# Kernel optimization log

Hardware: AMD Instinct MI355X
Metric: run time of the kernel (lower is better)

## Reference

```python
import jax, jax.numpy as jnp
import numpy as np

B, C, H, W = 32, 512, 256, 14
NSEL = 7  # 7 even columns (0,2,..,12) on even rows, 7 odd columns (1,3,..,13) on odd rows


def setup_inputs() -> dict:
    key = jax.random.key(0)
    kx, kp = jax.random.split(key)
    x = jax.random.normal(kx, (B, C, H, W), dtype=jnp.float32)
    # per-(batch,row) random permutation of the 7 selected columns
    pkeys = jax.random.split(kp, B * H)
    perms = jax.vmap(lambda k: jax.random.permutation(k, NSEL))(pkeys)
    perms = perms.reshape(B, H, NSEL).astype(jnp.int32)
    return {"x": x, "perms": perms}


def reference(x, perms):
    # Even rows shuffle columns {0,2,...,12}; odd rows shuffle {1,3,...,13}.
    # Column of the j-th selected element on row h: 2*j + (h % 2).
    parity = (jnp.arange(H) % 2).astype(jnp.int32)[None, :, None]      # [1,H,1]
    dst = 2 * jnp.arange(NSEL, dtype=jnp.int32)[None, None, :] + parity  # [1,H,7] -> broadcast [B,H,7]
    dst = jnp.broadcast_to(dst, (B, H, NSEL))
    src = 2 * perms + parity                                            # [B,H,7]
    # Build a per-(b,h) column remap: identity, with dst <- src on shuffled slots.
    colmap = jnp.broadcast_to(jnp.arange(W, dtype=jnp.int32), (B, H, W))
    bi = jnp.arange(B, dtype=jnp.int32)[:, None, None]
    hi = jnp.arange(H, dtype=jnp.int32)[None, :, None]
    colmap = colmap.at[bi, hi, dst].set(src)                            # [B,H,W]
    # Single vectorized gather along the width axis, broadcast over channels.
    idx = jnp.broadcast_to(colmap[:, None, :, :], (B, C, H, W))
    return jnp.take_along_axis(x, idx, axis=3)
```

## Files before the change

### kernel.cpp

```cpp
#include <hip/hip_runtime.h>


#define TILE_ROWS   512
#define TILE_FLOATS (TILE_ROWS * 14)
#define WAVE_ROWS   128
#define WAVE_VEC4   448

#define GLOAD_LDS16(gp, lp)                                                   \
    __builtin_amdgcn_global_load_lds(                                         \
        (const __attribute__((address_space(1))) void*)(gp),                  \
        (__attribute__((address_space(3))) void*)(lp), 16, 0, 0)

__global__ __launch_bounds__(256, 5) void GSRS_shuffle_wave_kernel(
    const float* __restrict__ x,
    const int* __restrict__ perms,
    float* __restrict__ out)
{
    __shared__ float tile[TILE_FLOATS];
    __shared__ unsigned char cmap[256][16];

    const unsigned tid  = threadIdx.x;
    const unsigned lane = tid & 63u;
    const unsigned wv   = tid >> 6;
    const unsigned tb   = blockIdx.x;
    const unsigned base = tb * TILE_FLOATS;
    const unsigned row0 = tb * TILE_ROWS;
    const unsigned b    = row0 >> 17;

    const float4* xv = reinterpret_cast<const float4*>(x + base);
    float4*       tv = reinterpret_cast<float4*>(tile);
    const unsigned q0 = wv * WAVE_VEC4 + lane;
#pragma unroll
    for (int i = 0; i < 7; ++i)
        GLOAD_LDS16(xv + q0 + i * 64, tv + q0 + i * 64);

    {
        const unsigned r0 = wv * WAVE_ROWS + 2u * lane;
        const unsigned h0 = r0 & 255u;
        const int* pr = perms + b * 1792u + h0 * 7u;
        int pm[14];
#pragma unroll
        for (int j = 0; j < 14; ++j) pm[j] = pr[j];
#pragma unroll
        for (int r = 0; r < 2; ++r) {
            const unsigned h = h0 + r;
            const unsigned p = h & 1u;
            union { unsigned char c[16]; uint4 v; } u;
#pragma unroll
            for (int w14 = 0; w14 < 14; ++w14) {
                unsigned src;
                if (((unsigned)w14 & 1u) == p)
                    src = 2u * (unsigned)pm[r * 7 + (w14 >> 1)] + p;
                else
                    src = (unsigned)w14;
                u.c[w14] = (unsigned char)src;
            }
            u.c[14] = 0; u.c[15] = 0;
            *reinterpret_cast<uint4*>(&cmap[h][0]) = u.v;
        }
    }

    asm volatile("s_waitcnt vmcnt(0) lgkmcnt(0)" ::: "memory");

    float4* ov = reinterpret_cast<float4*>(out + base);
#pragma unroll
    for (int i = 0; i < 7; ++i) {
        const unsigned q  = q0 + i * 64;
        unsigned lo   = q * 4u;
        unsigned lrow = lo / 14u;
        unsigned w14  = lo - lrow * 14u;
        float v[4];
#pragma unroll
        for (int k4 = 0; k4 < 4; ++k4) {
            const unsigned h   = lrow & 255u;
            const unsigned src = cmap[h][w14];
            v[k4] = tile[lrow * 14u + src];
            if (++w14 == 14u) { w14 = 0u; ++lrow; }
        }
        ov[q] = make_float4(v[0], v[1], v[2], v[3]);
    }
}

extern "C" void kernel_launch(void* const* d_in, const int* in_sizes, int n_in,
                              void* d_out, int out_size, void* d_ws, size_t ws_size,
                              hipStream_t stream) {
    const float* x     = (const float*)d_in[0];
    const int*   perms = (const int*)d_in[1];
    float*       out   = (float*)d_out;

    hipLaunchKernelGGL(GSRS_shuffle_wave_kernel, dim3(8192), dim3(256), 0, stream,
                       x, perms, out);
}
```

Before: 86.70 us.

## Process four tiles per block with register-prefetched next tile

Each block now handles four consecutive 512-row tiles from the same batch. The next tile is prefetched into registers while the current tile is permuted from LDS and stored. Direct global-to-LDS loads are replaced by ordinary register loads followed by LDS writes, and the column map is built once per block, so per-block setup is amortized and load latency overlaps with the shuffle. The costs are higher register pressure, an extra register-to-LDS write, and a quarter as many blocks, which could hurt latency hiding on a kernel that is already bandwidth-bound.

```diff
diff --git a/kernel.cpp b/kernel.cpp
--- a/kernel.cpp
+++ b/kernel.cpp
@@ -3,15 +3,11 @@
 
 #define TILE_ROWS   512
 #define TILE_FLOATS (TILE_ROWS * 14)
-#define WAVE_ROWS   128
-#define WAVE_VEC4   448
+#define TILE_V4     (TILE_FLOATS / 4)
+#define WAVE_V4     448
+#define TILES_PER_BLOCK 4
 
-#define GLOAD_LDS16(gp, lp)                                                   \
-    __builtin_amdgcn_global_load_lds(                                         \
-        (const __attribute__((address_space(1))) void*)(gp),                  \
-        (__attribute__((address_space(3))) void*)(lp), 16, 0, 0)
-
-__global__ __launch_bounds__(256, 5) void GSRS_shuffle_wave_kernel(
+__global__ __launch_bounds__(256, 5) void GSRS_shuffle_pipe_kernel(
     const float* __restrict__ x,
     const int* __restrict__ perms,
     float* __restrict__ out)
@@ -22,37 +18,36 @@
     const unsigned tid  = threadIdx.x;
     const unsigned lane = tid & 63u;
     const unsigned wv   = tid >> 6;
-    const unsigned tb   = blockIdx.x;
-    const unsigned base = tb * TILE_FLOATS;
-    const unsigned row0 = tb * TILE_ROWS;
-    const unsigned b    = row0 >> 17;
+    const unsigned bid  = blockIdx.x;
+    const unsigned t0   = bid * TILES_PER_BLOCK;
+    const unsigned b    = t0 >> 8;
 
-    const float4* xv = reinterpret_cast<const float4*>(x + base);
-    float4*       tv = reinterpret_cast<float4*>(tile);
-    const unsigned q0 = wv * WAVE_VEC4 + lane;
+    const unsigned q0 = wv * WAVE_V4 + lane;
+    float4* tv = reinterpret_cast<float4*>(tile);
+
+    const float4* xv = reinterpret_cast<const float4*>(x);
+    float4 r[7];
 #pragma unroll
     for (int i = 0; i < 7; ++i)
-        GLOAD_LDS16(xv + q0 + i * 64, tv + q0 + i * 64);
+        r[i] = xv[(size_t)t0 * TILE_V4 + q0 + i * 64];
 
     {
-        const unsigned r0 = wv * WAVE_ROWS + 2u * lane;
+        const unsigned r0 = wv * 128u + 2u * lane;
         const unsigned h0 = r0 & 255u;
         const int* pr = perms + b * 1792u + h0 * 7u;
         int pm[14];
 #pragma unroll
         for (int j = 0; j < 14; ++j) pm[j] = pr[j];
 #pragma unroll
-        for (int r = 0; r < 2; ++r) {
-            const unsigned h = h0 + r;
+        for (int rr = 0; rr < 2; ++rr) {
+            const unsigned h = h0 + rr;
             const unsigned p = h & 1u;
             union { unsigned char c[16]; uint4 v; } u;
 #pragma unroll
             for (int w14 = 0; w14 < 14; ++w14) {
-                unsigned src;
-                if (((unsigned)w14 & 1u) == p)
-                    src = 2u * (unsigned)pm[r * 7 + (w14 >> 1)] + p;
-                else
-                    src = (unsigned)w14;
+                unsigned src = (((unsigned)w14 & 1u) == p)
+                    ? 2u * (unsigned)pm[rr * 7 + (w14 >> 1)] + p
+                    : (unsigned)w14;
                 u.c[w14] = (unsigned char)src;
             }
             u.c[14] = 0; u.c[15] = 0;
@@ -60,24 +55,41 @@
         }
     }
 
-    asm volatile("s_waitcnt vmcnt(0) lgkmcnt(0)" ::: "memory");
+#pragma unroll
+    for (int i = 0; i < 7; ++i)
+        tv[q0 + i * 64] = r[i];
 
-    float4* ov = reinterpret_cast<float4*>(out + base);
 #pragma unroll
-    for (int i = 0; i < 7; ++i) {
-        const unsigned q  = q0 + i * 64;
-        unsigned lo   = q * 4u;
-        unsigned lrow = lo / 14u;
-        unsigned w14  = lo - lrow * 14u;
-        float v[4];
+    for (int t = 0; t < TILES_PER_BLOCK; ++t) {
+        if (t + 1 < TILES_PER_BLOCK) {
 #pragma unroll
-        for (int k4 = 0; k4 < 4; ++k4) {
-            const unsigned h   = lrow & 255u;
-            const unsigned src = cmap[h][w14];
-            v[k4] = tile[lrow * 14u + src];
-            if (++w14 == 14u) { w14 = 0u; ++lrow; }
+            for (int i = 0; i < 7; ++i)
+                r[i] = xv[(size_t)(t0 + t + 1) * TILE_V4 + q0 + i * 64];
         }
-        ov[q] = make_float4(v[0], v[1], v[2], v[3]);
+
+        float4* ov = reinterpret_cast<float4*>(out) + (size_t)(t0 + t) * TILE_V4;
+#pragma unroll
+        for (int i = 0; i < 7; ++i) {
+            const unsigned q  = q0 + i * 64;
+            unsigned lo   = q * 4u;
+            unsigned lrow = lo / 14u;
+            unsigned w14  = lo - lrow * 14u;
+            float v[4];
+#pragma unroll
+            for (int k4 = 0; k4 < 4; ++k4) {
+                const unsigned h   = lrow & 255u;
+                const unsigned src = cmap[h][w14];
+                v[k4] = tile[lrow * 14u + src];
+                if (++w14 == 14u) { w14 = 0u; ++lrow; }
+            }
+            ov[q] = make_float4(v[0], v[1], v[2], v[3]);
+        }
+
+        if (t + 1 < TILES_PER_BLOCK) {
+#pragma unroll
+            for (int i = 0; i < 7; ++i)
+                tv[q0 + i * 64] = r[i];
+        }
     }
 }
 
@@ -88,6 +100,6 @@
     const int*   perms = (const int*)d_in[1];
     float*       out   = (float*)d_out;
 
-    hipLaunchKernelGGL(GSRS_shuffle_wave_kernel, dim3(8192), dim3(256), 0, stream,
+    hipLaunchKernelGGL(GSRS_shuffle_pipe_kernel, dim3(2048), dim3(256), 0, stream,
                        x, perms, out);
 }
```

New measurement: 100.1 us. 15.5% more time.
